# Kernel optimization log

Measured on AMD Instinct MI355X. Metric: run time of the kernel, lower is better.

The kernel has to match this reference:

```python
import jax, jax.numpy as jnp
import numpy as np

N, L, S, D, H, DK = 4, 2048, 2048, 1024, 16, 64


def setup_inputs() -> dict:
    key = jax.random.key(0)
    kq, kk, kv, kwq, kwo = jax.random.split(key, 5)
    Q = jax.random.normal(kq, (N, L, D), dtype=jnp.float32)
    K = jax.random.normal(kk, (N, S, D), dtype=jnp.float32)
    V = jax.random.normal(kv, (N, S, D), dtype=jnp.float32)
    # per-head query projection weights (the source reuses Lq for K and V too)
    Wq = jax.random.normal(kwq, (H, DK, D), dtype=jnp.float32) * (D ** -0.5)
    # output projection Lo: Linear(h*dv -> Dv), weight shape (out, in)
    Wo = jax.random.normal(kwo, (D, H * DK), dtype=jnp.float32) * ((H * DK) ** -0.5)
    return {"Q": Q, "K": K, "V": V, "Wq": Wq, "Wo": Wo}


def reference(Q, K, V, Wq, Wo):
    dk = Wq.shape[1]
    # Faithful to source: ALL of q, k, v are projected with the Lq weights.
    q = jnp.einsum('nld,hkd->hnlk', Q, Wq)   # (H,N,L,dk)
    k = jnp.einsum('nsd,hkd->hnsk', K, Wq)   # (H,N,S,dk)
    v = jnp.einsum('nsd,hkd->hnsk', V, Wq)   # (H,N,S,dk)
    scale = jnp.asarray(dk, Q.dtype) ** 0.5
    scores = jnp.einsum('hnlk,hnsk->hnls', q, k) / scale  # (H,N,L,S)
    # Faithful to F.softmax(dot) with no dim on a 3D tensor: torch picks dim=0
    # (the batch axis N); here that is axis=1 of the head-stacked (H,N,L,S).
    attn = jax.nn.softmax(scores, axis=1)
    heads = jnp.einsum('hnls,hnsk->hnlk', attn, v)        # (H,N,L,dk)
    # concat heads along last dim -> (N,L,H*dk)
    heads = jnp.transpose(heads, (1, 2, 0, 3)).reshape(Q.shape[0], Q.shape[1], -1)
    return heads @ Wo.T  # (N,L,Dv)
```

## Files before the change

### kernel.cpp

```cpp
#include <hip/hip_runtime.h>
#include <hip/hip_bf16.h>

typedef __attribute__((ext_vector_type(8))) short short8;
typedef __attribute__((ext_vector_type(4))) short short4v;
typedef __attribute__((ext_vector_type(4))) float float4v;

#define DEVI static __device__ __forceinline__

#if __has_builtin(__builtin_amdgcn_exp2f)
#define EXP2(x) __builtin_amdgcn_exp2f(x)
#else
#define EXP2(x) exp2f(x)
#endif

DEVI unsigned short f2bf(float f) {
  unsigned int u = __builtin_bit_cast(unsigned int, f);
  u += 0x7fffu + ((u >> 16) & 1u);
  return (unsigned short)(u >> 16);
}

DEVI short8 pack8(float4v a, float4v b) {
  struct P4 { __hip_bfloat162 x, y, z, w; } t;
  t.x = __float22bfloat162_rn(make_float2(a[0], a[1]));
  t.y = __float22bfloat162_rn(make_float2(a[2], a[3]));
  t.z = __float22bfloat162_rn(make_float2(b[0], b[1]));
  t.w = __float22bfloat162_rn(make_float2(b[2], b[3]));
  short8 r;
  __builtin_memcpy(&r, &t, 16);
  return r;
}

DEVI short4v pack4(float a, float b, float c, float d) {
  struct P2 { __hip_bfloat162 x, y; } t;
  t.x = __float22bfloat162_rn(make_float2(a, b));
  t.y = __float22bfloat162_rn(make_float2(c, d));
  short4v r;
  __builtin_memcpy(&r, &t, 8);
  return r;
}

DEVI void gload16(const void* src, void* lds_dst) {
  __builtin_amdgcn_global_load_lds(
      (const __attribute__((address_space(1))) void*)src,
      (__attribute__((address_space(3))) void*)lds_dst, 16, 0, 0);
}

template<int AF32, int CMODE>
__global__ __launch_bounds__(256, 2)
void gemm_bt128(const void* __restrict__ Ap, const float* __restrict__ Bp,
                void* __restrict__ Cp, int M, int Nc, int Kd, float oscale)
{
  __shared__ alignas(16) short As[2][128 * 40];
  __shared__ alignas(16) short Bs[2][128 * 40];

  const int tid = threadIdx.x;
  const int lane = tid & 63;
  const int wid = tid >> 6;
  const int rl = lane & 15;
  const int g = lane >> 4;
  const int bm = blockIdx.x * 128;
  const int bn = blockIdx.y * 128;
  const int wm = (wid >> 1) * 64;
  const int wn = (wid & 1) * 64;
  const int srow = tid >> 1;
  const int k0 = (tid & 1) * 16;

  float4v acc[4][4];
#pragma unroll
  for (int i = 0; i < 4; ++i)
#pragma unroll
    for (int j = 0; j < 4; ++j) acc[i][j] = (float4v)(0.0f);

  const float* Af = (const float*)Ap;
  const unsigned short* Ab = (const unsigned short*)Ap;

  float4v afr[4], bfr[4];
  short8 ah[2], bh[2];

  const int NK = Kd >> 5;

  auto loadA = [&](int ks) {
    size_t base = (size_t)(bm + srow) * Kd + ks * 32 + k0;
    if constexpr (AF32 != 0) {
      afr[0] = *(const float4v*)(Af + base);
      afr[1] = *(const float4v*)(Af + base + 4);
      afr[2] = *(const float4v*)(Af + base + 8);
      afr[3] = *(const float4v*)(Af + base + 12);
    } else {
      ah[0] = *(const short8*)(Ab + base);
      ah[1] = *(const short8*)(Ab + base + 8);
    }
  };
  auto loadB = [&](int ks) {
    size_t base = (size_t)(bn + srow) * Kd + ks * 32 + k0;
    bfr[0] = *(const float4v*)(Bp + base);
    bfr[1] = *(const float4v*)(Bp + base + 4);
    bfr[2] = *(const float4v*)(Bp + base + 8);
    bfr[3] = *(const float4v*)(Bp + base + 12);
  };
  auto packAB = [&]() {
    if constexpr (AF32 != 0) {
      ah[0] = pack8(afr[0], afr[1]);
      ah[1] = pack8(afr[2], afr[3]);
    }
    bh[0] = pack8(bfr[0], bfr[1]);
    bh[1] = pack8(bfr[2], bfr[3]);
  };
  auto writeLDS = [&](int b) {
    *(short8*)(As[b] + srow * 40 + k0)     = ah[0];
    *(short8*)(As[b] + srow * 40 + k0 + 8) = ah[1];
    *(short8*)(Bs[b] + srow * 40 + k0)     = bh[0];
    *(short8*)(Bs[b] + srow * 40 + k0 + 8) = bh[1];
  };

  loadA(0);
  loadB(0);
  packAB();
  writeLDS(0);
  __syncthreads();

  for (int ks = 0; ks < NK; ++ks) {
    if (ks + 1 < NK) { loadA(ks + 1); loadB(ks + 1); }

    const int b = ks & 1;
    short8 a8[4], b8[4];
#pragma unroll
    for (int mt = 0; mt < 4; ++mt)
      a8[mt] = *(const short8*)(As[b] + (wm + mt * 16 + rl) * 40 + 8 * g);
#pragma unroll
    for (int nt = 0; nt < 4; ++nt)
      b8[nt] = *(const short8*)(Bs[b] + (wn + nt * 16 + rl) * 40 + 8 * g);
#pragma unroll
    for (int mt = 0; mt < 4; ++mt)
#pragma unroll
      for (int nt = 0; nt < 4; ++nt)
        acc[mt][nt] = __builtin_amdgcn_mfma_f32_16x16x32_bf16(a8[mt], b8[nt], acc[mt][nt], 0, 0, 0);

    if (ks + 1 < NK) {
      packAB();
      writeLDS(b ^ 1);
    }
    __syncthreads();
  }

#pragma unroll
  for (int mt = 0; mt < 4; ++mt)
#pragma unroll
    for (int nt = 0; nt < 4; ++nt) {
      const int col = bn + wn + nt * 16 + rl;
      const int row0 = bm + wm + mt * 16 + 4 * g;
      if constexpr (CMODE == 1) {
        float* C = (float*)Cp;
#pragma unroll
        for (int r = 0; r < 4; ++r)
          C[(size_t)(row0 + r) * Nc + col] = acc[mt][nt][r];
      } else if constexpr (CMODE == 0) {
        unsigned short* C = (unsigned short*)Cp;
#pragma unroll
        for (int r = 0; r < 4; ++r)
          C[(size_t)(row0 + r) * Nc + col] = f2bf(acc[mt][nt][r] * oscale);
      } else {
        unsigned short* C = (unsigned short*)Cp;
        short4v w = pack4(acc[mt][nt][0], acc[mt][nt][1], acc[mt][nt][2], acc[mt][nt][3]);
        const int u = row0 & 31;
        const int pm = (row0 & ~31) | (((u >> 2) & 3) << 3) | (((u >> 4) & 1) << 2);
        *(short4v*)(C + (size_t)col * M + pm) = w;
      }
    }
}

__global__ __launch_bounds__(512, 2)
void attn_bn(const unsigned short* __restrict__ qb,
             const unsigned short* __restrict__ kb,
             const unsigned short* __restrict__ vtb,
             unsigned short* __restrict__ hb)
{
  __shared__ alignas(128) char smem[131072];

  const int tid = threadIdx.x;
  const int lane = tid & 63;
  const int wid = tid >> 6;
  const int rl = lane & 15;
  const int g = lane >> 4;
  const int h = blockIdx.y;
  const int l0 = blockIdx.x * 128 + wid * 16;

  short8 qf[4][2];
#pragma unroll
  for (int n = 0; n < 4; ++n)
#pragma unroll
    for (int dh = 0; dh < 2; ++dh)
      qf[n][dh] = *(const short8*)(qb + (size_t)(n * 2048 + l0 + rl) * 1024 + h * 64 + dh * 32 + 8 * g);

  float4v ha[4][4];
#pragma unroll
  for (int n = 0; n < 4; ++n)
#pragma unroll
    for (int t = 0; t < 4; ++t) ha[n][t] = (float4v)(0.0f);

  const size_t koff0 = ((size_t)(wid * 2048) + (size_t)(lane >> 3)) * 1024
                     + (size_t)(h * 64) + (size_t)(((lane & 7) ^ (lane >> 3)) * 8);
  const size_t voff0 = ((size_t)(h * 64) + (size_t)(lane >> 2)) * 8192
                     + (size_t)((wid - 4) * 2048)
                     + (size_t)((((lane & 3) ^ ((lane >> 3) & 3)) * 8));

  auto stage = [&](int step, int b) {
    if (wid < 4) {
      char* kdst = smem + b * 32768 + wid * 4096;
      const unsigned short* ksrc = kb + koff0 + (size_t)step * 32 * 1024;
#pragma unroll
      for (int ii = 0; ii < 4; ++ii)
        gload16(ksrc + ii * 8192, kdst + ii * 1024);
    } else {
      char* vdst = smem + b * 32768 + 16384 + (wid - 4) * 4096;
      const unsigned short* vsrc = vtb + voff0 + (size_t)step * 32;
#pragma unroll
      for (int ii = 0; ii < 4; ++ii)
        gload16(vsrc + (size_t)ii * 16 * 8192, vdst + ii * 1024);
    }
  };

  stage(0, 0);
  stage(1, 1);
  stage(2, 2);
  asm volatile("s_waitcnt vmcnt(8)" ::: "memory");
  __builtin_amdgcn_s_barrier();

  const unsigned voffr = ((unsigned)(g ^ ((rl >> 1) & 3))) << 4;

  for (int to = 0; to < 16; ++to) {
#pragma unroll
    for (int ti = 0; ti < 4; ++ti) {
      const int t = to * 4 + ti;
      char* kbase = smem + ti * 32768;
      char* vbase = kbase + 16384;

      float4v sc[4][2];
#pragma unroll
      for (int n = 0; n < 4; ++n) {
        char* kn = kbase + n * 4096;
#pragma unroll
        for (int ss = 0; ss < 2; ++ss) {
          const int srw = ss * 16 + rl;
          const unsigned sw = ((unsigned)(srw & 7)) << 4;
          short8 kf0 = *(const short8*)(kn + srw * 128 + ((16u * (unsigned)g) ^ sw));
          short8 kf1 = *(const short8*)(kn + srw * 128 + ((64u + 16u * (unsigned)g) ^ sw));
          float4v c = (float4v)(0.0f);
          c = __builtin_amdgcn_mfma_f32_16x16x32_bf16(kf0, qf[n][0], c, 0, 0, 0);
          c = __builtin_amdgcn_mfma_f32_16x16x32_bf16(kf1, qf[n][1], c, 0, 0, 0);
          sc[n][ss] = c;
        }
      }

      float ex[4][2][4];
#pragma unroll
      for (int ss = 0; ss < 2; ++ss) {
#pragma unroll
        for (int n = 0; n < 4; ++n)
#pragma unroll
          for (int r = 0; r < 4; ++r)
            ex[n][ss][r] = EXP2(fminf(sc[n][ss][r], 24.0f));
#pragma unroll
        for (int r = 0; r < 4; ++r) {
          float inv = __builtin_amdgcn_rcpf((ex[0][ss][r] + ex[1][ss][r])
                                          + (ex[2][ss][r] + ex[3][ss][r]) + 1e-30f);
          ex[0][ss][r] *= inv; ex[1][ss][r] *= inv;
          ex[2][ss][r] *= inv; ex[3][ss][r] *= inv;
        }
      }
      short8 pf8[4];
#pragma unroll
      for (int n = 0; n < 4; ++n) {
        float4v e0 = {ex[n][0][0], ex[n][0][1], ex[n][0][2], ex[n][0][3]};
        float4v e1 = {ex[n][1][0], ex[n][1][1], ex[n][1][2], ex[n][1][3]};
        pf8[n] = pack8(e0, e1);
      }

#pragma unroll
      for (int n = 0; n < 4; ++n) {
        char* vn = vbase + n * 4096;
#pragma unroll
        for (int t4 = 0; t4 < 4; ++t4) {
          short8 va = *(const short8*)(vn + (t4 * 16 + rl) * 64 + voffr);
          ha[n][t4] = __builtin_amdgcn_mfma_f32_16x16x32_bf16(va, pf8[n], ha[n][t4], 0, 0, 0);
        }
      }

      if (t + 3 < 64) stage(t + 3, (ti + 3) & 3);
      asm volatile("s_waitcnt vmcnt(8)" ::: "memory");
      __builtin_amdgcn_s_barrier();
    }
  }

#pragma unroll
  for (int n = 0; n < 4; ++n)
#pragma unroll
    for (int tt = 0; tt < 4; ++tt) {
      short4v w = pack4(ha[n][tt][0], ha[n][tt][1], ha[n][tt][2], ha[n][tt][3]);
      size_t off = (size_t)(n * 2048 + l0 + rl) * 1024 + h * 64 + tt * 16 + 4 * g;
      *(short4v*)(hb + off) = w;
    }
}

extern "C" void kernel_launch(void* const* d_in, const int* in_sizes, int n_in,
                              void* d_out, int out_size, void* d_ws, size_t ws_size,
                              hipStream_t stream)
{
  const float* Q  = (const float*)d_in[0];
  const float* K  = (const float*)d_in[1];
  const float* V  = (const float*)d_in[2];
  const float* Wq = (const float*)d_in[3];
  const float* Wo = (const float*)d_in[4];

  unsigned short* qb = (unsigned short*)d_ws;
  unsigned short* kw = qb + (size_t)8192 * 1024;
  unsigned short* vt = kw + (size_t)8192 * 1024;
  unsigned short* hw = qb;

  const float CS = 0.18033688011112042f;

  dim3 gg(64, 8), bb(256);
  gemm_bt128<1, 0><<<gg, bb, 0, stream>>>(Q, Wq, qb, 8192, 1024, 1024, CS);
  gemm_bt128<1, 0><<<gg, bb, 0, stream>>>(K, Wq, kw, 8192, 1024, 1024, 1.0f);
  gemm_bt128<1, 2><<<gg, bb, 0, stream>>>(V, Wq, vt, 8192, 1024, 1024, 1.0f);
  attn_bn<<<dim3(16, 16), dim3(512), 0, stream>>>(qb, kw, vt, hw);
  gemm_bt128<0, 1><<<gg, bb, 0, stream>>>(hw, Wo, (float*)d_out, 8192, 1024, 1024, 1.0f);
}
```

Baseline: 260.7 us.

## Pre-convert weights to bf16 and stage GEMM tiles via direct global-to-LDS loads

Adds a small kernel that converts Wq and Wo to bf16 once per call, so every GEMM block reads the B operand at half the bytes and skips per-tile packing. The bf16 B tiles, and the A tiles for the output projection, are now copied straight into LDS with asynchronous global_load_lds instead of going through registers. The LDS row stride drops to 32 shorts, with no padding. This also drops the fminf clamp before exp2 in attention. Risks are LDS bank conflicts from the unpadded stride, two extra launches, and possible overflow in exp2 without the clamp.

```diff
diff --git a/kernel.cpp b/kernel.cpp
--- a/kernel.cpp
+++ b/kernel.cpp
@@ -45,13 +45,25 @@
       (__attribute__((address_space(3))) void*)lds_dst, 16, 0, 0);
 }
 
+__global__ __launch_bounds__(256)
+void cvt_bf16(const float* __restrict__ in, unsigned short* __restrict__ out, int n8)
+{
+  int i = blockIdx.x * 256 + threadIdx.x;
+  if (i < n8) {
+    float4v a = *(const float4v*)(in + (size_t)i * 8);
+    float4v b = *(const float4v*)(in + (size_t)i * 8 + 4);
+    *(short8*)(out + (size_t)i * 8) = pack8(a, b);
+  }
+}
+
 template<int AF32, int CMODE>
 __global__ __launch_bounds__(256, 2)
-void gemm_bt128(const void* __restrict__ Ap, const float* __restrict__ Bp,
+void gemm_bt128(const void* __restrict__ Ap, const unsigned short* __restrict__ Bp,
                 void* __restrict__ Cp, int M, int Nc, int Kd, float oscale)
 {
-  __shared__ alignas(16) short As[2][128 * 40];
-  __shared__ alignas(16) short Bs[2][128 * 40];
+  constexpr int AS = AF32 ? 40 : 32;
+  __shared__ alignas(16) short As[2][128 * AS];
+  __shared__ alignas(16) short Bs[2][128 * 32];
 
   const int tid = threadIdx.x;
   const int lane = tid & 63;
@@ -74,72 +86,74 @@
   const float* Af = (const float*)Ap;
   const unsigned short* Ab = (const unsigned short*)Ap;
 
-  float4v afr[4], bfr[4];
-  short8 ah[2], bh[2];
+  float4v afr[4];
+  short8 ah[2];
 
   const int NK = Kd >> 5;
 
+  const int grow = (tid >> 2) + 0;
+  const int gchk = tid & 3;
+
+  auto stageB = [&](int ks, int b) {
+#pragma unroll
+    for (int j = 0; j < 2; ++j) {
+      const unsigned short* src = Bp + (size_t)(bn + grow + j * 64) * Kd + ks * 32 + gchk * 8;
+      gload16(src, (char*)Bs[b] + j * 4096 + wid * 1024);
+    }
+  };
+  auto stageA16 = [&](int ks, int b) {
+#pragma unroll
+    for (int j = 0; j < 2; ++j) {
+      const unsigned short* src = Ab + (size_t)(bm + grow + j * 64) * Kd + ks * 32 + gchk * 8;
+      gload16(src, (char*)As[b] + j * 4096 + wid * 1024);
+    }
+  };
   auto loadA = [&](int ks) {
     size_t base = (size_t)(bm + srow) * Kd + ks * 32 + k0;
-    if constexpr (AF32 != 0) {
-      afr[0] = *(const float4v*)(Af + base);
-      afr[1] = *(const float4v*)(Af + base + 4);
-      afr[2] = *(const float4v*)(Af + base + 8);
-      afr[3] = *(const float4v*)(Af + base + 12);
-    } else {
-      ah[0] = *(const short8*)(Ab + base);
-      ah[1] = *(const short8*)(Ab + base + 8);
-    }
-  };
-  auto loadB = [&](int ks) {
-    size_t base = (size_t)(bn + srow) * Kd + ks * 32 + k0;
-    bfr[0] = *(const float4v*)(Bp + base);
-    bfr[1] = *(const float4v*)(Bp + base + 4);
-    bfr[2] = *(const float4v*)(Bp + base + 8);
-    bfr[3] = *(const float4v*)(Bp + base + 12);
-  };
-  auto packAB = [&]() {
-    if constexpr (AF32 != 0) {
-      ah[0] = pack8(afr[0], afr[1]);
-      ah[1] = pack8(afr[2], afr[3]);
-    }
-    bh[0] = pack8(bfr[0], bfr[1]);
-    bh[1] = pack8(bfr[2], bfr[3]);
-  };
-  auto writeLDS = [&](int b) {
+    afr[0] = *(const float4v*)(Af + base);
+    afr[1] = *(const float4v*)(Af + base + 4);
+    afr[2] = *(const float4v*)(Af + base + 8);
+    afr[3] = *(const float4v*)(Af + base + 12);
+  };
+  auto packWriteA = [&](int b) {
+    ah[0] = pack8(afr[0], afr[1]);
+    ah[1] = pack8(afr[2], afr[3]);
     *(short8*)(As[b] + srow * 40 + k0)     = ah[0];
     *(short8*)(As[b] + srow * 40 + k0 + 8) = ah[1];
-    *(short8*)(Bs[b] + srow * 40 + k0)     = bh[0];
-    *(short8*)(Bs[b] + srow * 40 + k0 + 8) = bh[1];
-  };
-
-  loadA(0);
-  loadB(0);
-  packAB();
-  writeLDS(0);
+  };
+
+  stageB(0, 0);
+  if constexpr (AF32 != 0) {
+    loadA(0);
+    packWriteA(0);
+  } else {
+    stageA16(0, 0);
+  }
   __syncthreads();
 
   for (int ks = 0; ks < NK; ++ks) {
-    if (ks + 1 < NK) { loadA(ks + 1); loadB(ks + 1); }
-
     const int b = ks & 1;
+    if (ks + 1 < NK) {
+      stageB(ks + 1, b ^ 1);
+      if constexpr (AF32 != 0) loadA(ks + 1);
+      else stageA16(ks + 1, b ^ 1);
+    }
+
     short8 a8[4], b8[4];
 #pragma unroll
     for (int mt = 0; mt < 4; ++mt)
-      a8[mt] = *(const short8*)(As[b] + (wm + mt * 16 + rl) * 40 + 8 * g);
+      a8[mt] = *(const short8*)(As[b] + (wm + mt * 16 + rl) * AS + 8 * g);
 #pragma unroll
     for (int nt = 0; nt < 4; ++nt)
-      b8[nt] = *(const short8*)(Bs[b] + (wn + nt * 16 + rl) * 40 + 8 * g);
+      b8[nt] = *(const short8*)(Bs[b] + (wn + nt * 16 + rl) * 32 + 8 * g);
 #pragma unroll
     for (int mt = 0; mt < 4; ++mt)
 #pragma unroll
       for (int nt = 0; nt < 4; ++nt)
         acc[mt][nt] = __builtin_amdgcn_mfma_f32_16x16x32_bf16(a8[mt], b8[nt], acc[mt][nt], 0, 0, 0);
 
-    if (ks + 1 < NK) {
-      packAB();
-      writeLDS(b ^ 1);
-    }
+    if constexpr (AF32 != 0)
+      if (ks + 1 < NK) packWriteA(b ^ 1);
     __syncthreads();
   }
 
@@ -259,7 +273,7 @@
         for (int n = 0; n < 4; ++n)
 #pragma unroll
           for (int r = 0; r < 4; ++r)
-            ex[n][ss][r] = EXP2(fminf(sc[n][ss][r], 24.0f));
+            ex[n][ss][r] = EXP2(sc[n][ss][r]);
 #pragma unroll
         for (int r = 0; r < 4; ++r) {
           float inv = __builtin_amdgcn_rcpf((ex[0][ss][r] + ex[1][ss][r])
@@ -312,17 +326,21 @@
   const float* Wq = (const float*)d_in[3];
   const float* Wo = (const float*)d_in[4];
 
-  unsigned short* qb = (unsigned short*)d_ws;
-  unsigned short* kw = qb + (size_t)8192 * 1024;
-  unsigned short* vt = kw + (size_t)8192 * 1024;
-  unsigned short* hw = qb;
+  unsigned short* qb  = (unsigned short*)d_ws;
+  unsigned short* kw  = qb + (size_t)8192 * 1024;
+  unsigned short* vt  = kw + (size_t)8192 * 1024;
+  unsigned short* wqb = vt + (size_t)8192 * 1024;
+  unsigned short* wob = wqb + (size_t)1024 * 1024;
+  unsigned short* hw  = qb;
 
   const float CS = 0.18033688011112042f;
 
   dim3 gg(64, 8), bb(256);
-  gemm_bt128<1, 0><<<gg, bb, 0, stream>>>(Q, Wq, qb, 8192, 1024, 1024, CS);
-  gemm_bt128<1, 0><<<gg, bb, 0, stream>>>(K, Wq, kw, 8192, 1024, 1024, 1.0f);
-  gemm_bt128<1, 2><<<gg, bb, 0, stream>>>(V, Wq, vt, 8192, 1024, 1024, 1.0f);
+  cvt_bf16<<<512, 256, 0, stream>>>(Wq, wqb, 131072);
+  cvt_bf16<<<512, 256, 0, stream>>>(Wo, wob, 131072);
+  gemm_bt128<1, 0><<<gg, bb, 0, stream>>>(Q, wqb, qb, 8192, 1024, 1024, CS);
+  gemm_bt128<1, 0><<<gg, bb, 0, stream>>>(K, wqb, kw, 8192, 1024, 1024, 1.0f);
+  gemm_bt128<1, 2><<<gg, bb, 0, stream>>>(V, wqb, vt, 8192, 1024, 1024, 1.0f);
   attn_bn<<<dim3(16, 16), dim3(512), 0, stream>>>(qb, kw, vt, hw);
-  gemm_bt128<0, 1><<<gg, bb, 0, stream>>>(hw, Wo, (float*)d_out, 8192, 1024, 1024, 1.0f);
-}
+  gemm_bt128<0, 1><<<gg, bb, 0, stream>>>(hw, wob, (float*)d_out, 8192, 1024, 1024, 1.0f);
+}
```

After: 239.2 us. 1.09x faster.
